# Optimization experiments

Hardware: AMD Instinct MI355X
Metric: run time of the kernel (lower is better)

## Reference

```python
import jax, jax.numpy as jnp
import numpy as np

B, N, D, H = 2, 512, 256, 8
HD = D // H
DFF = 4 * D
EPS = 1e-5


def layer_norm(x, g, b):
    m = jnp.mean(x, axis=-1, keepdims=True)
    v = jnp.mean(jnp.square(x - m), axis=-1, keepdims=True)
    return (x - m) * jax.lax.rsqrt(v + EPS) * g + b


def setup_inputs() -> dict:
    key = jax.random.key(0)
    ks = jax.random.split(key, 16)
    s = 0.02
    return {
        "node_features": jax.random.normal(ks[0], (B, N, D), jnp.float32),
        "edge_features": jax.random.normal(ks[1], (B, N, N, D), jnp.float32),
        "adjacency_mask": jax.random.randint(ks[2], (B, N, N), 0, 2, jnp.int32),
        "node_norm_g": jnp.ones((D,), jnp.float32),
        "node_norm_b": jnp.zeros((D,), jnp.float32),
        "edge_norm_g": jnp.ones((D,), jnp.float32),
        "edge_norm_b": jnp.zeros((D,), jnp.float32),
        "Wq": jax.random.normal(ks[3], (D, D), jnp.float32) * s,
        "bq": jnp.zeros((D,), jnp.float32),
        "Wk": jax.random.normal(ks[4], (D, D), jnp.float32) * s,
        "bk": jnp.zeros((D,), jnp.float32),
        "Wv": jax.random.normal(ks[5], (D, D), jnp.float32) * s,
        "bv": jnp.zeros((D,), jnp.float32),
        "Wo": jax.random.normal(ks[6], (D, D), jnp.float32) * s,
        "bo": jnp.zeros((D,), jnp.float32),
        "We": jax.random.normal(ks[7], (D, H), jnp.float32) * s,
        "be": jnp.zeros((H,), jnp.float32),
        "ff_norm_g": jnp.ones((D,), jnp.float32),
        "ff_norm_b": jnp.zeros((D,), jnp.float32),
        "W1": jax.random.normal(ks[8], (D, DFF), jnp.float32) * s,
        "b1": jnp.zeros((DFF,), jnp.float32),
        "W2": jax.random.normal(ks[9], (DFF, D), jnp.float32) * s,
        "b2": jnp.zeros((D,), jnp.float32),
    }


def reference(node_features, edge_features, adjacency_mask,
              node_norm_g, node_norm_b, edge_norm_g, edge_norm_b,
              Wq, bq, Wk, bk, Wv, bv, Wo, bo, We, be,
              ff_norm_g, ff_norm_b, W1, b1, W2, b2):
    x = node_features
    nn_ = layer_norm(x, node_norm_g, node_norm_b)
    # project and split heads: (B, H, N, HD)
    q = (nn_ @ Wq + bq).reshape(B, N, H, HD).transpose(0, 2, 1, 3)
    k = (nn_ @ Wk + bk).reshape(B, N, H, HD).transpose(0, 2, 1, 3)
    v = (nn_ @ Wv + bv).reshape(B, N, H, HD).transpose(0, 2, 1, 3)
    scores = jnp.einsum('bhnd,bhmd->bhnm', q, k) / jnp.sqrt(jnp.float32(HD))
    # edge bias: LayerNorm over D then Linear(D->H), move H first
    eb = layer_norm(edge_features, edge_norm_g, edge_norm_b) @ We + be  # (B,N,N,H)
    scores = scores + eb.transpose(0, 3, 1, 2)
    scores = jnp.where(adjacency_mask[:, None, :, :] == 0, -jnp.inf, scores)
    attn = jax.nn.softmax(scores, axis=-1)
    out = jnp.einsum('bhnm,bhmd->bhnd', attn, v)
    out = out.transpose(0, 2, 1, 3).reshape(B, N, D) @ Wo + bo
    x = x + out
    # feedforward (dropout is identity at inference)
    h = layer_norm(x, ff_norm_g, ff_norm_b)
    h = jax.nn.gelu(h @ W1 + b1, approximate=False) @ W2 + b2
    return x + h
```

## Files before the change

### kernel.cpp

```cpp
#include <hip/hip_runtime.h>
#include <hip/hip_bf16.h>

typedef unsigned int uint;

constexpr float EPS_ = 1e-5f;

#define DEV __device__ __forceinline__

DEV float gelu_(float x){ return 0.5f*x*(1.f + erff(x*0.70710678118654752f)); }

DEV float blockSum256(float v, float* red){
    #pragma unroll
    for (int o = 32; o >= 1; o >>= 1) v += __shfl_xor(v, o);
    int t = threadIdx.x;
    __syncthreads();
    if ((t & 63) == 0) red[t >> 6] = v;
    __syncthreads();
    return red[0]+red[1]+red[2]+red[3];
}

__global__ __launch_bounds__(256) void k_setup(
    const float* __restrict__ g, const float* __restrict__ b,
    const float* __restrict__ We, const float* __restrict__ be,
    float* __restrict__ GW, float* __restrict__ A, float* __restrict__ C)
{
    const int d = threadIdx.x;
    __shared__ float redA[256*8];
    __shared__ float redC[256*8];
    float gd = g[d], bd = b[d];
    #pragma unroll
    for (int h = 0; h < 8; ++h) {
        float w = We[d*8+h];
        float gw = gd*w;
        GW[d*8+h] = gw;
        redA[d*8+h] = gw;
        redC[d*8+h] = bd*w;
    }
    __syncthreads();
    for (int s = 128; s >= 1; s >>= 1) {
        if (d < s) {
            #pragma unroll
            for (int h = 0; h < 8; ++h) {
                redA[d*8+h] += redA[(d+s)*8+h];
                redC[d*8+h] += redC[(d+s)*8+h];
            }
        }
        __syncthreads();
    }
    if (d < 8) {
        A[d] = redA[d];
        C[d] = redC[d] + be[d];
    }
}

__global__ __launch_bounds__(256) void k_qkv(
    const float* __restrict__ x,
    const float* __restrict__ g, const float* __restrict__ bta,
    const float* __restrict__ Wq, const float* __restrict__ bq,
    const float* __restrict__ Wk, const float* __restrict__ bk,
    const float* __restrict__ Wv, const float* __restrict__ bv,
    float* __restrict__ q, float* __restrict__ k, float* __restrict__ v)
{
    const int row = blockIdx.x;
    const int t = threadIdx.x;
    __shared__ float sx[256];
    __shared__ float red[4];
    float xv = x[row*256 + t];
    float s1 = blockSum256(xv, red);
    float s2 = blockSum256(xv*xv, red);
    float m = s1 * (1.f/256.f);
    float rinv = rsqrtf(s2*(1.f/256.f) - m*m + EPS_);
    sx[t] = (xv - m) * rinv * g[t] + bta[t];
    __syncthreads();
    float aq = bq[t], ak = bk[t], av = bv[t];
    for (int d = 0; d < 256; ++d) {
        float s = sx[d];
        aq = fmaf(s, Wq[d*256 + t], aq);
        ak = fmaf(s, Wk[d*256 + t], ak);
        av = fmaf(s, Wv[d*256 + t], av);
    }
    q[row*256 + t] = aq;
    k[row*256 + t] = ak;
    v[row*256 + t] = av;
}

__global__ __launch_bounds__(256) void k_eattn(
    const float4* __restrict__ ep,
    const int*   __restrict__ msk,
    const float* __restrict__ GW, const float* __restrict__ Avec, const float* __restrict__ Cvec,
    const float* __restrict__ qg, const float* __restrict__ kg, const float* __restrict__ vg,
    float* __restrict__ ao)
{
    __shared__ float slds[256*33];
    __shared__ float sgw[2048];
    __shared__ float sac[16];
    __shared__ float sb[8*512];
    __shared__ float sp[8*512];
    __shared__ float sqv[256];
    __shared__ float sden[8];
    const int t = threadIdx.x;
    const int bi = blockIdx.x;
    const int b = bi >> 9;
    #pragma unroll
    for (int kk = 0; kk < 8; ++kk) sgw[kk*256 + t] = GW[kk*256 + t];
    if (t < 8) { sac[t] = Avec[t]; sac[8 + t] = Cvec[t]; }
    sqv[t] = qg[(size_t)bi*256 + t] * 0.17677669529663687f;
    __syncthreads();

    for (int half = 0; half < 2; ++half) {
        const long long rowBase = ((long long)bi << 9) + (half << 8);
        float sum = 0.f, ssq = 0.f;
        float S[8] = {0.f,0.f,0.f,0.f,0.f,0.f,0.f,0.f};
        for (int c = 0; c < 8; ++c) {
            #pragma unroll
            for (int kk = 0; kk < 8; ++kk) {
                int l2 = (kk << 8) + t;
                int r = l2 >> 3, u = l2 & 7;
                float4 val = ep[(rowBase + r)*64 + (c << 3) + u];
                float* dst = &slds[r*33 + (u << 2)];
                dst[0] = val.x; dst[1] = val.y; dst[2] = val.z; dst[3] = val.w;
            }
            __syncthreads();
            const float* srow = &slds[t*33];
            const int dbase = c << 5;
            #pragma unroll 4
            for (int j = 0; j < 32; ++j) {
                float e = srow[j];
                const float* g0 = &sgw[(dbase + j) << 3];
                sum += e;
                ssq = fmaf(e, e, ssq);
                #pragma unroll
                for (int h = 0; h < 8; ++h) S[h] = fmaf(e, g0[h], S[h]);
            }
            __syncthreads();
        }
        const float m = sum * (1.f/256.f);
        const float rinv = rsqrtf(ssq*(1.f/256.f) - m*m + EPS_);
        const float mb = (msk[rowBase + t] == 0) ? -1e30f : 0.f;
        const int jrow = (half << 8) + t;
        #pragma unroll
        for (int h = 0; h < 8; ++h)
            sb[h*512 + jrow] = rinv * (S[h] - m * sac[h]) + sac[8 + h] + mb;
    }
    __syncthreads();

    const int h = t >> 5, l = t & 31;
    const float* kb = kg + ((size_t)b << 9)*256 + h*32;
    const float4* qr = (const float4*)(sqv + h*32);
    float sc[16];
    float pmax = -3.0e38f;
    #pragma unroll
    for (int mi = 0; mi < 16; ++mi) {
        const int j = l + (mi << 5);
        const float4* kr = (const float4*)(kb + (size_t)j*256);
        float a = 0.f;
        #pragma unroll
        for (int w = 0; w < 8; ++w) {
            float4 kv = kr[w], qv = qr[w];
            a += kv.x*qv.x + kv.y*qv.y + kv.z*qv.z + kv.w*qv.w;
        }
        float s0 = a + sb[h*512 + j];
        sc[mi] = s0;
        pmax = fmaxf(pmax, s0);
    }
    #pragma unroll
    for (int o = 16; o >= 1; o >>= 1) pmax = fmaxf(pmax, __shfl_xor(pmax, o));
    float psum = 0.f;
    #pragma unroll
    for (int mi = 0; mi < 16; ++mi) {
        float p = __expf(sc[mi] - pmax);
        sp[h*512 + l + (mi << 5)] = p;
        psum += p;
    }
    #pragma unroll
    for (int o = 16; o >= 1; o >>= 1) psum += __shfl_xor(psum, o);
    if (l == 0) sden[h] = psum;
    __syncthreads();

    const float* vb = vg + ((size_t)b << 9)*256 + t;
    const float* spr = &sp[h*512];
    float a0 = 0.f, a1 = 0.f, a2 = 0.f, a3 = 0.f;
    for (int j = 0; j < 512; j += 4) {
        a0 = fmaf(spr[j],   vb[(size_t)(j)*256],   a0);
        a1 = fmaf(spr[j+1], vb[(size_t)(j+1)*256], a1);
        a2 = fmaf(spr[j+2], vb[(size_t)(j+2)*256], a2);
        a3 = fmaf(spr[j+3], vb[(size_t)(j+3)*256], a3);
    }
    ao[(size_t)bi*256 + t] = (a0+a1+a2+a3) / sden[h];
}

__global__ __launch_bounds__(256) void k_proj(
    const float* __restrict__ at, const float* __restrict__ Wo,
    const float* __restrict__ bo, const float* __restrict__ x,
    float* __restrict__ x1)
{
    const int row = blockIdx.x, t = threadIdx.x;
    __shared__ float sa[256];
    sa[t] = at[row*256 + t];
    __syncthreads();
    float acc = bo[t];
    for (int d = 0; d < 256; ++d) acc = fmaf(sa[d], Wo[d*256 + t], acc);
    x1[row*256 + t] = acc + x[row*256 + t];
}

__global__ __launch_bounds__(256) void k_ff(
    const float* __restrict__ x1, const float* __restrict__ g,
    const float* __restrict__ bb,
    const float* __restrict__ W1, const float* __restrict__ b1,
    const float* __restrict__ W2, const float* __restrict__ b2,
    float* __restrict__ out)
{
    const int row = blockIdx.x, t = threadIdx.x;
    __shared__ float sh[256];
    __shared__ float sf[1024];
    __shared__ float red[4];
    float xv = x1[row*256 + t];
    float s1 = blockSum256(xv, red);
    float s2 = blockSum256(xv*xv, red);
    float m = s1*(1.f/256.f);
    float rinv = rsqrtf(s2*(1.f/256.f) - m*m + EPS_);
    sh[t] = (xv - m)*rinv*g[t] + bb[t];
    __syncthreads();
    float a0 = b1[t], a1 = b1[t+256], a2 = b1[t+512], a3 = b1[t+768];
    for (int d = 0; d < 256; ++d) {
        float s = sh[d];
        const float* wr = W1 + d*1024 + t;
        a0 = fmaf(s, wr[0],   a0);
        a1 = fmaf(s, wr[256], a1);
        a2 = fmaf(s, wr[512], a2);
        a3 = fmaf(s, wr[768], a3);
    }
    sf[t]     = gelu_(a0);
    sf[t+256] = gelu_(a1);
    sf[t+512] = gelu_(a2);
    sf[t+768] = gelu_(a3);
    __syncthreads();
    float acc = b2[t];
    for (int kk = 0; kk < 1024; ++kk) acc = fmaf(sf[kk], W2[kk*256 + t], acc);
    out[row*256 + t] = acc + xv;
}

extern "C" void kernel_launch(void* const* d_in, const int* in_sizes, int n_in,
                              void* d_out, int out_size, void* d_ws, size_t ws_size,
                              hipStream_t stream) {
    const float* x   = (const float*)d_in[0];
    const float* ef  = (const float*)d_in[1];
    const int*   am  = (const int*)d_in[2];
    const float* ng  = (const float*)d_in[3];
    const float* nb  = (const float*)d_in[4];
    const float* eg  = (const float*)d_in[5];
    const float* ebb = (const float*)d_in[6];
    const float* Wq  = (const float*)d_in[7];
    const float* bq  = (const float*)d_in[8];
    const float* Wk  = (const float*)d_in[9];
    const float* bk  = (const float*)d_in[10];
    const float* Wv  = (const float*)d_in[11];
    const float* bv  = (const float*)d_in[12];
    const float* Wo  = (const float*)d_in[13];
    const float* bo  = (const float*)d_in[14];
    const float* We  = (const float*)d_in[15];
    const float* be  = (const float*)d_in[16];
    const float* fg  = (const float*)d_in[17];
    const float* fb  = (const float*)d_in[18];
    const float* W1  = (const float*)d_in[19];
    const float* b1  = (const float*)d_in[20];
    const float* W2  = (const float*)d_in[21];
    const float* b2  = (const float*)d_in[22];

    float* ws  = (float*)d_ws;
    float* GW  = ws;
    float* Av  = ws + 2048;
    float* Cv  = ws + 2064;
    float* q   = ws + 4096;
    float* k   = q  + 262144;
    float* v   = k  + 262144;
    float* ao  = v  + 262144;
    float* x1  = ao + 262144;

    hipLaunchKernelGGL(k_setup, dim3(1), dim3(256), 0, stream, eg, ebb, We, be, GW, Av, Cv);
    hipLaunchKernelGGL(k_qkv, dim3(1024), dim3(256), 0, stream,
                       x, ng, nb, Wq, bq, Wk, bk, Wv, bv, q, k, v);
    hipLaunchKernelGGL(k_eattn, dim3(1024), dim3(256), 0, stream,
                       (const float4*)ef, am, GW, Av, Cv, q, k, v, ao);
    hipLaunchKernelGGL(k_proj, dim3(1024), dim3(256), 0, stream, ao, Wo, bo, x, x1);
    hipLaunchKernelGGL(k_ff, dim3(1024), dim3(256), 0, stream,
                       x1, fg, fb, W1, b1, W2, b2, (float*)d_out);
}
```

Before: 330.9 us.

## Process four rows per block in dense projection and FFN kernels

The QKV, output-projection and feedforward kernels now compute four rows per block. LayerNorm runs per wavefront with shuffle reductions, and the normalized activations are stored transposed so each weight element loaded from memory is reused for four rows. Grid sizes drop accordingly. The edge-bias loop also reads its projected weights with float4 loads. This trades much less weight traffic for fewer blocks, which means less parallelism and more registers per thread.

```diff
diff --git a/kernel.cpp b/kernel.cpp
--- a/kernel.cpp
+++ b/kernel.cpp
@@ -8,16 +8,6 @@
 #define DEV __device__ __forceinline__
 
 DEV float gelu_(float x){ return 0.5f*x*(1.f + erff(x*0.70710678118654752f)); }
-
-DEV float blockSum256(float v, float* red){
-    #pragma unroll
-    for (int o = 32; o >= 1; o >>= 1) v += __shfl_xor(v, o);
-    int t = threadIdx.x;
-    __syncthreads();
-    if ((t & 63) == 0) red[t >> 6] = v;
-    __syncthreads();
-    return red[0]+red[1]+red[2]+red[3];
-}
 
 __global__ __launch_bounds__(256) void k_setup(
     const float* __restrict__ g, const float* __restrict__ b,
@@ -61,27 +51,47 @@
     const float* __restrict__ Wv, const float* __restrict__ bv,
     float* __restrict__ q, float* __restrict__ k, float* __restrict__ v)
 {
-    const int row = blockIdx.x;
     const int t = threadIdx.x;
-    __shared__ float sx[256];
-    __shared__ float red[4];
-    float xv = x[row*256 + t];
-    float s1 = blockSum256(xv, red);
-    float s2 = blockSum256(xv*xv, red);
-    float m = s1 * (1.f/256.f);
-    float rinv = rsqrtf(s2*(1.f/256.f) - m*m + EPS_);
-    sx[t] = (xv - m) * rinv * g[t] + bta[t];
-    __syncthreads();
-    float aq = bq[t], ak = bk[t], av = bv[t];
+    const int wid = t >> 6, l = t & 63;
+    const int r0 = blockIdx.x << 2;
+    __shared__ float sxT[256*4];
+    {
+        const int row = r0 + wid;
+        const float4 xv4 = ((const float4*)x)[row*64 + l];
+        float s  = xv4.x + xv4.y + xv4.z + xv4.w;
+        float q2 = xv4.x*xv4.x + xv4.y*xv4.y + xv4.z*xv4.z + xv4.w*xv4.w;
+        #pragma unroll
+        for (int o = 32; o >= 1; o >>= 1) { s += __shfl_xor(s, o); q2 += __shfl_xor(q2, o); }
+        const float m = s * (1.f/256.f);
+        const float rinv = rsqrtf(q2*(1.f/256.f) - m*m + EPS_);
+        const float4 g4 = ((const float4*)g)[l];
+        const float4 b4 = ((const float4*)bta)[l];
+        sxT[(4*l+0)*4 + wid] = (xv4.x - m)*rinv*g4.x + b4.x;
+        sxT[(4*l+1)*4 + wid] = (xv4.y - m)*rinv*g4.y + b4.y;
+        sxT[(4*l+2)*4 + wid] = (xv4.z - m)*rinv*g4.z + b4.z;
+        sxT[(4*l+3)*4 + wid] = (xv4.w - m)*rinv*g4.w + b4.w;
+    }
+    __syncthreads();
+    const float bqv = bq[t], bkv = bk[t], bvv = bv[t];
+    float4 AQ = make_float4(bqv,bqv,bqv,bqv);
+    float4 AK = make_float4(bkv,bkv,bkv,bkv);
+    float4 AV = make_float4(bvv,bvv,bvv,bvv);
     for (int d = 0; d < 256; ++d) {
-        float s = sx[d];
-        aq = fmaf(s, Wq[d*256 + t], aq);
-        ak = fmaf(s, Wk[d*256 + t], ak);
-        av = fmaf(s, Wv[d*256 + t], av);
-    }
-    q[row*256 + t] = aq;
-    k[row*256 + t] = ak;
-    v[row*256 + t] = av;
+        const float4 s4 = *((const float4*)&sxT[d*4]);
+        const float wq = Wq[d*256 + t], wk = Wk[d*256 + t], wv = Wv[d*256 + t];
+        AQ.x = fmaf(s4.x, wq, AQ.x); AQ.y = fmaf(s4.y, wq, AQ.y);
+        AQ.z = fmaf(s4.z, wq, AQ.z); AQ.w = fmaf(s4.w, wq, AQ.w);
+        AK.x = fmaf(s4.x, wk, AK.x); AK.y = fmaf(s4.y, wk, AK.y);
+        AK.z = fmaf(s4.z, wk, AK.z); AK.w = fmaf(s4.w, wk, AK.w);
+        AV.x = fmaf(s4.x, wv, AV.x); AV.y = fmaf(s4.y, wv, AV.y);
+        AV.z = fmaf(s4.z, wv, AV.z); AV.w = fmaf(s4.w, wv, AV.w);
+    }
+    q[(r0+0)*256 + t] = AQ.x; q[(r0+1)*256 + t] = AQ.y;
+    q[(r0+2)*256 + t] = AQ.z; q[(r0+3)*256 + t] = AQ.w;
+    k[(r0+0)*256 + t] = AK.x; k[(r0+1)*256 + t] = AK.y;
+    k[(r0+2)*256 + t] = AK.z; k[(r0+3)*256 + t] = AK.w;
+    v[(r0+0)*256 + t] = AV.x; v[(r0+1)*256 + t] = AV.y;
+    v[(r0+2)*256 + t] = AV.z; v[(r0+3)*256 + t] = AV.w;
 }
 
 __global__ __launch_bounds__(256) void k_eattn(
@@ -126,11 +136,14 @@
             #pragma unroll 4
             for (int j = 0; j < 32; ++j) {
                 float e = srow[j];
-                const float* g0 = &sgw[(dbase + j) << 3];
+                const float4* g4p = (const float4*)&sgw[(dbase + j) << 3];
+                const float4 ga = g4p[0], gb = g4p[1];
                 sum += e;
                 ssq = fmaf(e, e, ssq);
-                #pragma unroll
-                for (int h = 0; h < 8; ++h) S[h] = fmaf(e, g0[h], S[h]);
+                S[0] = fmaf(e, ga.x, S[0]); S[1] = fmaf(e, ga.y, S[1]);
+                S[2] = fmaf(e, ga.z, S[2]); S[3] = fmaf(e, ga.w, S[3]);
+                S[4] = fmaf(e, gb.x, S[4]); S[5] = fmaf(e, gb.y, S[5]);
+                S[6] = fmaf(e, gb.z, S[6]); S[7] = fmaf(e, gb.w, S[7]);
             }
             __syncthreads();
         }
@@ -194,13 +207,30 @@
     const float* __restrict__ bo, const float* __restrict__ x,
     float* __restrict__ x1)
 {
-    const int row = blockIdx.x, t = threadIdx.x;
-    __shared__ float sa[256];
-    sa[t] = at[row*256 + t];
-    __syncthreads();
-    float acc = bo[t];
-    for (int d = 0; d < 256; ++d) acc = fmaf(sa[d], Wo[d*256 + t], acc);
-    x1[row*256 + t] = acc + x[row*256 + t];
+    const int t = threadIdx.x;
+    const int wid = t >> 6, l = t & 63;
+    const int r0 = blockIdx.x << 2;
+    __shared__ float saT[256*4];
+    {
+        const float4 a4 = ((const float4*)at)[(r0 + wid)*64 + l];
+        saT[(4*l+0)*4 + wid] = a4.x;
+        saT[(4*l+1)*4 + wid] = a4.y;
+        saT[(4*l+2)*4 + wid] = a4.z;
+        saT[(4*l+3)*4 + wid] = a4.w;
+    }
+    __syncthreads();
+    const float bov = bo[t];
+    float4 A = make_float4(bov,bov,bov,bov);
+    for (int d = 0; d < 256; ++d) {
+        const float4 s4 = *((const float4*)&saT[d*4]);
+        const float wo = Wo[d*256 + t];
+        A.x = fmaf(s4.x, wo, A.x); A.y = fmaf(s4.y, wo, A.y);
+        A.z = fmaf(s4.z, wo, A.z); A.w = fmaf(s4.w, wo, A.w);
+    }
+    x1[(r0+0)*256 + t] = A.x + x[(r0+0)*256 + t];
+    x1[(r0+1)*256 + t] = A.y + x[(r0+1)*256 + t];
+    x1[(r0+2)*256 + t] = A.z + x[(r0+2)*256 + t];
+    x1[(r0+3)*256 + t] = A.w + x[(r0+3)*256 + t];
 }
 
 __global__ __launch_bounds__(256) void k_ff(
@@ -210,34 +240,63 @@
     const float* __restrict__ W2, const float* __restrict__ b2,
     float* __restrict__ out)
 {
-    const int row = blockIdx.x, t = threadIdx.x;
-    __shared__ float sh[256];
-    __shared__ float sf[1024];
-    __shared__ float red[4];
-    float xv = x1[row*256 + t];
-    float s1 = blockSum256(xv, red);
-    float s2 = blockSum256(xv*xv, red);
-    float m = s1*(1.f/256.f);
-    float rinv = rsqrtf(s2*(1.f/256.f) - m*m + EPS_);
-    sh[t] = (xv - m)*rinv*g[t] + bb[t];
-    __syncthreads();
-    float a0 = b1[t], a1 = b1[t+256], a2 = b1[t+512], a3 = b1[t+768];
+    const int t = threadIdx.x;
+    const int wid = t >> 6, l = t & 63;
+    const int r0 = blockIdx.x << 2;
+    __shared__ float shT[256*4];
+    __shared__ float sfT[1024*4];
+    {
+        const int row = r0 + wid;
+        const float4 xv4 = ((const float4*)x1)[row*64 + l];
+        float s  = xv4.x + xv4.y + xv4.z + xv4.w;
+        float q2 = xv4.x*xv4.x + xv4.y*xv4.y + xv4.z*xv4.z + xv4.w*xv4.w;
+        #pragma unroll
+        for (int o = 32; o >= 1; o >>= 1) { s += __shfl_xor(s, o); q2 += __shfl_xor(q2, o); }
+        const float m = s * (1.f/256.f);
+        const float rinv = rsqrtf(q2*(1.f/256.f) - m*m + EPS_);
+        const float4 g4 = ((const float4*)g)[l];
+        const float4 b4 = ((const float4*)bb)[l];
+        shT[(4*l+0)*4 + wid] = (xv4.x - m)*rinv*g4.x + b4.x;
+        shT[(4*l+1)*4 + wid] = (xv4.y - m)*rinv*g4.y + b4.y;
+        shT[(4*l+2)*4 + wid] = (xv4.z - m)*rinv*g4.z + b4.z;
+        shT[(4*l+3)*4 + wid] = (xv4.w - m)*rinv*g4.w + b4.w;
+    }
+    __syncthreads();
+    const float bc0 = b1[t], bc1 = b1[t+256], bc2 = b1[t+512], bc3 = b1[t+768];
+    float4 A0 = make_float4(bc0,bc0,bc0,bc0);
+    float4 A1 = make_float4(bc1,bc1,bc1,bc1);
+    float4 A2 = make_float4(bc2,bc2,bc2,bc2);
+    float4 A3 = make_float4(bc3,bc3,bc3,bc3);
     for (int d = 0; d < 256; ++d) {
-        float s = sh[d];
+        const float4 s4 = *((const float4*)&shT[d*4]);
         const float* wr = W1 + d*1024 + t;
-        a0 = fmaf(s, wr[0],   a0);
-        a1 = fmaf(s, wr[256], a1);
-        a2 = fmaf(s, wr[512], a2);
-        a3 = fmaf(s, wr[768], a3);
-    }
-    sf[t]     = gelu_(a0);
-    sf[t+256] = gelu_(a1);
-    sf[t+512] = gelu_(a2);
-    sf[t+768] = gelu_(a3);
-    __syncthreads();
-    float acc = b2[t];
-    for (int kk = 0; kk < 1024; ++kk) acc = fmaf(sf[kk], W2[kk*256 + t], acc);
-    out[row*256 + t] = acc + xv;
+        const float w0 = wr[0], w1 = wr[256], w2 = wr[512], w3 = wr[768];
+        A0.x = fmaf(s4.x, w0, A0.x); A0.y = fmaf(s4.y, w0, A0.y);
+        A0.z = fmaf(s4.z, w0, A0.z); A0.w = fmaf(s4.w, w0, A0.w);
+        A1.x = fmaf(s4.x, w1, A1.x); A1.y = fmaf(s4.y, w1, A1.y);
+        A1.z = fmaf(s4.z, w1, A1.z); A1.w = fmaf(s4.w, w1, A1.w);
+        A2.x = fmaf(s4.x, w2, A2.x); A2.y = fmaf(s4.y, w2, A2.y);
+        A2.z = fmaf(s4.z, w2, A2.z); A2.w = fmaf(s4.w, w2, A2.w);
+        A3.x = fmaf(s4.x, w3, A3.x); A3.y = fmaf(s4.y, w3, A3.y);
+        A3.z = fmaf(s4.z, w3, A3.z); A3.w = fmaf(s4.w, w3, A3.w);
+    }
+    *((float4*)&sfT[(t      )*4]) = make_float4(gelu_(A0.x), gelu_(A0.y), gelu_(A0.z), gelu_(A0.w));
+    *((float4*)&sfT[(t +  256)*4]) = make_float4(gelu_(A1.x), gelu_(A1.y), gelu_(A1.z), gelu_(A1.w));
+    *((float4*)&sfT[(t +  512)*4]) = make_float4(gelu_(A2.x), gelu_(A2.y), gelu_(A2.z), gelu_(A2.w));
+    *((float4*)&sfT[(t +  768)*4]) = make_float4(gelu_(A3.x), gelu_(A3.y), gelu_(A3.z), gelu_(A3.w));
+    __syncthreads();
+    const float b2v = b2[t];
+    float4 AO = make_float4(b2v,b2v,b2v,b2v);
+    for (int kk = 0; kk < 1024; ++kk) {
+        const float4 s4 = *((const float4*)&sfT[kk*4]);
+        const float w = W2[kk*256 + t];
+        AO.x = fmaf(s4.x, w, AO.x); AO.y = fmaf(s4.y, w, AO.y);
+        AO.z = fmaf(s4.z, w, AO.z); AO.w = fmaf(s4.w, w, AO.w);
+    }
+    out[(r0+0)*256 + t] = AO.x + x1[(r0+0)*256 + t];
+    out[(r0+1)*256 + t] = AO.y + x1[(r0+1)*256 + t];
+    out[(r0+2)*256 + t] = AO.z + x1[(r0+2)*256 + t];
+    out[(r0+3)*256 + t] = AO.w + x1[(r0+3)*256 + t];
 }
 
 extern "C" void kernel_launch(void* const* d_in, const int* in_sizes, int n_in,
@@ -278,11 +337,11 @@
     float* x1  = ao + 262144;
 
     hipLaunchKernelGGL(k_setup, dim3(1), dim3(256), 0, stream, eg, ebb, We, be, GW, Av, Cv);
-    hipLaunchKernelGGL(k_qkv, dim3(1024), dim3(256), 0, stream,
+    hipLaunchKernelGGL(k_qkv, dim3(256), dim3(256), 0, stream,
                        x, ng, nb, Wq, bq, Wk, bk, Wv, bv, q, k, v);
     hipLaunchKernelGGL(k_eattn, dim3(1024), dim3(256), 0, stream,
                        (const float4*)ef, am, GW, Av, Cv, q, k, v, ao);
-    hipLaunchKernelGGL(k_proj, dim3(1024), dim3(256), 0, stream, ao, Wo, bo, x, x1);
-    hipLaunchKernelGGL(k_ff, dim3(1024), dim3(256), 0, stream,
+    hipLaunchKernelGGL(k_proj, dim3(256), dim3(256), 0, stream, ao, Wo, bo, x, x1);
+    hipLaunchKernelGGL(k_ff, dim3(256), dim3(256), 0, stream,
                        x1, fg, fb, W1, b1, W2, b2, (float*)d_out);
 }
```

After: 347.6 us. +5.1%, slower.
